# Kernel optimization log

Hardware: AMD Instinct MI355X
Metric: run time of the kernel (lower is better)

The kernel has to match this reference:

```python
import jax, jax.numpy as jnp
import numpy as np

B, T, D = 4, 2048, 2048
H, HD = 16, 128  # n_heads, head_dim; inner_dim = H*HD = 2048
SCALE = float(np.sqrt(HD))


def setup_inputs() -> dict:
    key = jax.random.key(0)
    kx, kq, kk, kv, ko = jax.random.split(key, 5)
    s = 0.02
    return {
        "x":  jax.random.normal(kx, (B, T, D), jnp.float32),
        "Wq": jax.random.normal(kq, (D, H * HD), jnp.float32) * s,
        "Wk": jax.random.normal(kk, (D, H * HD), jnp.float32) * s,
        "Wv": jax.random.normal(kv, (D, H * HD), jnp.float32) * s,
        "Wo": jax.random.normal(ko, (H * HD, D), jnp.float32) * s,
        "layer_idx": 0,
    }


def reference(x, Wq, Wk, Wv, Wo, layer_idx):
    # Cache starts empty and T <= max_cache_size, so cached_k/v == k/v and
    # T_cache == T; the sink/window mask reduces to a standard causal mask.
    b, t, _ = x.shape

    def split_heads(y):
        return y.reshape(b, t, H, HD).transpose(0, 2, 1, 3)  # (B,H,T,HD)

    q = split_heads(x @ Wq)
    k = split_heads(x @ Wk)
    v = split_heads(x @ Wv)

    scores = jnp.einsum('bhqd,bhkd->bhqk', q, k) / SCALE  # (B,H,T,T)
    q_idx = jnp.arange(t)
    k_idx = jnp.arange(t)
    causal = k_idx[None, :] <= q_idx[:, None]  # T_cache - T + q_idx == q_idx
    scores = jnp.where(causal[None, None], scores, -jnp.inf)
    w = jax.nn.softmax(scores, axis=-1)
    out = jnp.einsum('bhqk,bhkd->bhqd', w, v)
    out = out.transpose(0, 2, 1, 3).reshape(b, t, H * HD)
    return out @ Wo
```

## Files before the change

kernel.cpp:

```cpp
#include <hip/hip_runtime.h>
#include <hip/hip_bf16.h>
#include <stdint.h>

#define TT   2048
#define DD   2048
#define NH   16
#define NB   4
#define HDIM 128
#define MSZ  (NB * TT)
#define NQKV (3 * DD)
#define NT   32

typedef __attribute__((ext_vector_type(8))) __bf16 bf16x8;
typedef __attribute__((ext_vector_type(4))) float  f32x4;

typedef __attribute__((address_space(3))) void       lds_void;
typedef const __attribute__((address_space(1))) void g_void;

__device__ inline unsigned short f2bf(float f) {
  union { float f; unsigned u; } v; v.f = f;
  unsigned r = v.u + 0x7fffu + ((v.u >> 16) & 1u);
  return (unsigned short)(r >> 16);
}

__device__ inline unsigned short bfc(float f) {
  return __builtin_bit_cast(unsigned short, (__bf16)f);
}

__device__ inline void gload16(const void* g, void* l) {
  __builtin_amdgcn_global_load_lds((g_void*)g, (lds_void*)l, 16, 0, 0);
}

__device__ inline f32x4 mfma16(bf16x8 a, bf16x8 b, f32x4 c) {
  return __builtin_amdgcn_mfma_f32_16x16x32_bf16(a, b, c, 0, 0, 0);
}

#define RORMAX(x, C)                                                        \
  do {                                                                      \
    int pi_ = __builtin_amdgcn_mov_dpp(__builtin_bit_cast(int, x), (C),     \
                                       0xF, 0xF, true);                     \
    x = fmaxf(x, __builtin_bit_cast(float, pi_));                           \
  } while (0)

__global__ __launch_bounds__(256) void cvtx(const float* __restrict__ x,
                                            unsigned short* __restrict__ xb) {
  const int n4 = MSZ * DD / 4;
  for (int i = blockIdx.x * blockDim.x + threadIdx.x; i < n4;
       i += gridDim.x * blockDim.x) {
    float4 v = ((const float4*)x)[i];
    uint2 u;
    u.x = (unsigned)f2bf(v.x) | ((unsigned)f2bf(v.y) << 16);
    u.y = (unsigned)f2bf(v.z) | ((unsigned)f2bf(v.w) << 16);
    *(uint2*)&xb[(size_t)i * 4] = u;
  }
}

__global__ __launch_bounds__(256) void transW(const float* __restrict__ Wq,
                                              const float* __restrict__ Wk,
                                              const float* __restrict__ Wv,
                                              const float* __restrict__ Wo,
                                              unsigned short* __restrict__ Wtq,
                                              unsigned short* __restrict__ Wto) {
  __shared__ float tl[32][33];
  const int z = blockIdx.z;
  const float* W = (z == 0) ? Wq : (z == 1) ? Wk : (z == 2) ? Wv : Wo;
  unsigned short* outp = (z < 3) ? (Wtq + (size_t)z * DD * DD) : Wto;
  const int c = threadIdx.x & 31, r8 = threadIdx.x >> 5;
  const int k0 = blockIdx.y * 32, n0 = blockIdx.x * 32;
#pragma unroll
  for (int i = 0; i < 4; ++i)
    tl[r8 + 8 * i][c] = W[(size_t)(k0 + r8 + 8 * i) * DD + n0 + c];
  __syncthreads();
#pragma unroll
  for (int i = 0; i < 4; ++i)
    outp[(size_t)(n0 + r8 + 8 * i) * DD + k0 + c] = f2bf(tl[c][r8 + 8 * i]);
}

template <int EPI>
__global__ __launch_bounds__(512, 2) void gemm8(
    const unsigned short* __restrict__ A, const unsigned short* __restrict__ Bt,
    unsigned short* __restrict__ Qb, unsigned short* __restrict__ Kb,
    unsigned short* __restrict__ Vt, float* __restrict__ Cf) {
  __shared__ __align__(16) unsigned short As[2][2][8192];
  __shared__ __align__(16) unsigned short Bs[2][2][8192];
  const int tid = threadIdx.x;
  const int lane = tid & 63;
  const int w = tid >> 6;
  const int wm = w >> 2, wn = w & 3;
  const int l15 = lane & 15, g = lane >> 4;
  const int m0 = blockIdx.y * 256, n0 = blockIdx.x * 256;

  const int u  = (tid * 16) ^ (((tid >> 5) & 1) << 5);
  const int sr = (u >> 6) & 127;
  const int sc = (u & 63) >> 1;
  const unsigned short* sA0 = A  + (size_t)(m0 + sr) * DD + sc;
  const unsigned short* sA1 = A  + (size_t)(m0 + 128 + sr) * DD + sc;
  const unsigned short* sB0 = Bt + (size_t)(n0 + sr) * DD + sc;
  const unsigned short* sB1 = Bt + (size_t)(n0 + 128 + sr) * DD + sc;

  const int pA = ((l15 * 64 + g * 16) ^ (((l15 >> 3) & 1) << 5)) >> 1;
  const int pB = (wn & 1) * 2048 + pA;

  f32x4 acc[8][4] = {};

#define STAGE(kt, hf)                                                         \
  do {                                                                        \
    if ((kt) < NT) {                                                          \
      const unsigned short* s_ = (hf) == 0 ? sA0 : (hf) == 1 ? sA1            \
                                 : (hf) == 2 ? sB0 : sB1;                     \
      s_ += (kt) * 64;                                                        \
      unsigned short* d_ = ((hf) < 2 ? &As[(kt) & 1][(hf) & 1][0]             \
                                     : &Bs[(kt) & 1][(hf) & 1][0]) + tid * 8; \
      gload16(s_, d_);                                                        \
      gload16(s_ + 32, d_ + 4096);                                            \
    }                                                                         \
  } while (0)

#define MFMAQ(q)                                                              \
  do {                                                                        \
    __builtin_amdgcn_s_setprio(1);                                            \
    _Pragma("unroll") for (int n2 = 0; n2 < 2; ++n2)                          \
    _Pragma("unroll") for (int m2 = 0; m2 < 4; ++m2)                          \
    _Pragma("unroll") for (int kk = 0; kk < 2; ++kk)                          \
      acc[((q) & 1) * 4 + m2][((q) >> 1) * 2 + n2] =                          \
          mfma16(af[((q) & 1) * 4 + m2][kk], bq[((q) >> 1) * 2 + n2][kk],     \
                 acc[((q) & 1) * 4 + m2][((q) >> 1) * 2 + n2]);               \
    __builtin_amdgcn_s_setprio(0);                                            \
  } while (0)

#define TILE(t, buf)                                                          \
  do {                                                                        \
    const unsigned short* Ab = &As[buf][wm][0];                               \
    const unsigned short* Bb = &Bs[buf][wn >> 1][0];                          \
    bf16x8 af[8][2], bq[4][2];                                                \
    _Pragma("unroll") for (int m = 0; m < 8; ++m) {                           \
      af[m][0] = *(const bf16x8*)&Ab[pA + m * 512];                           \
      af[m][1] = *(const bf16x8*)&Ab[pA + m * 512 + 4096];                    \
    }                                                                         \
    _Pragma("unroll") for (int n = 0; n < 4; ++n) {                           \
      bq[n][0] = *(const bf16x8*)&Bb[pB + n * 512];                           \
      bq[n][1] = *(const bf16x8*)&Bb[pB + n * 512 + 4096];                    \
    }                                                                         \
    STAGE((t) + 1, 3);                                                        \
    __builtin_amdgcn_s_barrier();                                             \
    MFMAQ(0);                                                                 \
    asm volatile("s_waitcnt lgkmcnt(0)" ::: "memory");                        \
    __builtin_amdgcn_sched_barrier(0);                                        \
    __builtin_amdgcn_s_barrier();                                             \
    STAGE((t) + 2, 0);                                                        \
    __builtin_amdgcn_s_barrier();                                             \
    MFMAQ(1);                                                                 \
    __builtin_amdgcn_s_barrier();                                             \
    STAGE((t) + 2, 1);                                                        \
    __builtin_amdgcn_s_barrier();                                             \
    MFMAQ(2);                                                                 \
    __builtin_amdgcn_s_barrier();                                             \
    STAGE((t) + 2, 2);                                                        \
    __builtin_amdgcn_s_barrier();                                             \
    MFMAQ(3);                                                                 \
    asm volatile("s_waitcnt vmcnt(6)" ::: "memory");                          \
    __builtin_amdgcn_sched_barrier(0);                                        \
    __builtin_amdgcn_s_barrier();                                             \
  } while (0)

  STAGE(0, 0); STAGE(0, 1); STAGE(0, 2); STAGE(0, 3);
  STAGE(1, 0); STAGE(1, 1); STAGE(1, 2);
  asm volatile("s_waitcnt vmcnt(6)" ::: "memory");
  __builtin_amdgcn_sched_barrier(0);
  __builtin_amdgcn_s_barrier();

#pragma unroll 1
  for (int it = 0; it < NT / 2; ++it) {
    TILE(2 * it, 0);
    TILE(2 * it + 1, 1);
  }
#undef TILE
#undef MFMAQ
#undef STAGE

  const float QSCALE = 0.1275174308f;
#pragma unroll
  for (int m = 0; m < 8; ++m) {
#pragma unroll
    for (int n = 0; n < 4; ++n) {
      const int row0 = m0 + wm * 128 + m * 16 + 4 * g;
      const int col2 = wn * 64 + n * 16;
      const int col = n0 + col2 + l15;
      if (EPI == 1) {
#pragma unroll
        for (int r = 0; r < 4; ++r)
          Cf[(size_t)(row0 + r) * DD + col] = acc[m][n][r];
      } else {
        const int mat = n0 >> 11;
        const int h = ((n0 & 2047) + col2) >> 7;
        const int hd = (col2 & 127) + l15;
        if (mat == 0) {
#pragma unroll
          for (int r = 0; r < 4; ++r) {
            const int mm = row0 + r, b = mm >> 11, t = mm & 2047;
            Qb[((size_t)(b * NH + h) * TT + t) * HDIM + hd] =
                f2bf(acc[m][n][r] * QSCALE);
          }
        } else if (mat == 1) {
#pragma unroll
          for (int r = 0; r < 4; ++r) {
            const int mm = row0 + r, b = mm >> 11, t = mm & 2047;
            Kb[((size_t)(b * NH + h) * TT + t) * HDIM + hd] = f2bf(acc[m][n][r]);
          }
        } else {
          const int b = row0 >> 11, t = row0 & 2047;
          uint2 uu;
          uu.x = (unsigned)f2bf(acc[m][n][0]) | ((unsigned)f2bf(acc[m][n][1]) << 16);
          uu.y = (unsigned)f2bf(acc[m][n][2]) | ((unsigned)f2bf(acc[m][n][3]) << 16);
          *(uint2*)&Vt[((size_t)(b * NH + h) * HDIM + hd) * TT + t] = uu;
        }
      }
    }
  }
}

__global__ __launch_bounds__(256, 4) void attn(const unsigned short* __restrict__ Qb,
                                               const unsigned short* __restrict__ Kb,
                                               const unsigned short* __restrict__ Vt,
                                               unsigned short* __restrict__ O) {
  __shared__ __align__(16) unsigned short Ks[2][4096];
  __shared__ __align__(16) unsigned short Vs[2][4096];
  __shared__ __align__(16) unsigned short pl[4][16][40];

  const int bid = blockIdx.x;
  const int bx = (bid >> 3) & 15;
  const int bh = (bid & 7) + 8 * (bid >> 7);
  const int tid = threadIdx.x;
  const int w = tid >> 6;
  const int lane = tid & 63;
  const int l15 = lane & 15, g = lane >> 4;

  const unsigned short* Qh = Qb + (size_t)bh * TT * HDIM;
  const unsigned short* Kh = Kb + (size_t)bh * TT * HDIM;
  const unsigned short* Vh = Vt + (size_t)bh * HDIM * TT;
  const int b = bh >> 4, h = bh & 15;

  bf16x8 ones;
#pragma unroll
  for (int i = 0; i < 8; ++i) ones[i] = (__bf16)1.0f;

  const int kch = tid >> 5, krow = tid & 31;
  const int vc = tid >> 7, vrow = tid & 127;

  int buf = 0;
#pragma unroll 1
  for (int ph = 0; ph < 2; ++ph) {
    const int qt = ph ? bx : (31 - bx);
    const int q0 = qt * 64 + w * 16;
    const int nt = 2 * qt + 2;

    bf16x8 qf[4];
#pragma unroll
    for (int kc = 0; kc < 4; ++kc)
      qf[kc] = *(const bf16x8*)&Qh[(size_t)(q0 + l15) * HDIM + kc * 32 + g * 8];

    f32x4 o[8] = {};
    float mrow[4], lrow[4];
#pragma unroll
    for (int r = 0; r < 4; ++r) { mrow[r] = -1e30f; lrow[r] = 0.f; }

    {
      const int kv0 = 0;
      gload16(Kh + (size_t)(kv0 + krow) * HDIM + kch * 8,      &Ks[buf][(kch * 32 + krow) * 8]);
      gload16(Kh + (size_t)(kv0 + krow) * HDIM + (kch + 8) * 8,&Ks[buf][((kch + 8) * 32 + krow) * 8]);
      gload16(Vh + (size_t)vrow * TT + kv0 + vc * 8,           &Vs[buf][(vc * 128 + vrow) * 8]);
      gload16(Vh + (size_t)vrow * TT + kv0 + (vc + 2) * 8,     &Vs[buf][((vc + 2) * 128 + vrow) * 8]);
    }

#pragma unroll 1
    for (int t = 0; t < nt; ++t) {
      const int kv0 = t * 32;
      __syncthreads();
      if (t + 1 < nt) {
        const int kvn = kv0 + 32;
        gload16(Kh + (size_t)(kvn + krow) * HDIM + kch * 8,      &Ks[buf ^ 1][(kch * 32 + krow) * 8]);
        gload16(Kh + (size_t)(kvn + krow) * HDIM + (kch + 8) * 8,&Ks[buf ^ 1][((kch + 8) * 32 + krow) * 8]);
        gload16(Vh + (size_t)vrow * TT + kvn + vc * 8,           &Vs[buf ^ 1][(vc * 128 + vrow) * 8]);
        gload16(Vh + (size_t)vrow * TT + kvn + (vc + 2) * 8,     &Vs[buf ^ 1][((vc + 2) * 128 + vrow) * 8]);
      }

      if (kv0 <= q0 + 15) {
        f32x4 s0 = {}, s1 = {};
#pragma unroll
        for (int kc = 0; kc < 4; ++kc) {
          bf16x8 k0 = *(const bf16x8*)&Ks[buf][((kc * 4 + g) * 32 + l15) * 8];
          bf16x8 k1 = *(const bf16x8*)&Ks[buf][((kc * 4 + g) * 32 + 16 + l15) * 8];
          s0 = mfma16(qf[kc], k0, s0);
          s1 = mfma16(qf[kc], k1, s1);
        }
        float pmax[4];
#pragma unroll
        for (int r = 0; r < 4; ++r) {
          const int q = q0 + 4 * g + r;
          if (kv0 + l15 > q) s0[r] = -1e30f;
          if (kv0 + 16 + l15 > q) s1[r] = -1e30f;
          pmax[r] = fmaxf(s0[r], s1[r]);
        }
#pragma unroll
        for (int r = 0; r < 4; ++r) {
          RORMAX(pmax[r], 0x121);
          RORMAX(pmax[r], 0x122);
          RORMAX(pmax[r], 0x124);
          RORMAX(pmax[r], 0x128);
        }
        int need = 0;
#pragma unroll
        for (int r = 0; r < 4; ++r) need |= (pmax[r] > mrow[r] + 12.0f);
        if (__any(need)) {
          float al[4];
#pragma unroll
          for (int r = 0; r < 4; ++r) {
            const float mn = fmaxf(mrow[r], pmax[r]);
            al[r] = __builtin_amdgcn_exp2f(mrow[r] - mn);
            mrow[r] = mn;
            lrow[r] *= al[r];
          }
#pragma unroll
          for (int n8 = 0; n8 < 8; ++n8)
#pragma unroll
            for (int r = 0; r < 4; ++r) o[n8][r] *= al[r];
        }
#pragma unroll
        for (int r = 0; r < 4; ++r) {
          s0[r] = __builtin_amdgcn_exp2f(s0[r] - mrow[r]);
          s1[r] = __builtin_amdgcn_exp2f(s1[r] - mrow[r]);
        }

#pragma unroll
        for (int r = 0; r < 4; ++r) {
          pl[w][4 * g + r][l15] = bfc(s0[r]);
          pl[w][4 * g + r][16 + l15] = bfc(s1[r]);
        }
        bf16x8 pf = *(const bf16x8*)&pl[w][l15][g * 8];
        f32x4 z = {};
        f32x4 sm = mfma16(pf, ones, z);
#pragma unroll
        for (int r = 0; r < 4; ++r) lrow[r] += sm[r];
#pragma unroll
        for (int n8 = 0; n8 < 8; ++n8) {
          bf16x8 vf = *(const bf16x8*)&Vs[buf][(g * 128 + n8 * 16 + l15) * 8];
          o[n8] = mfma16(pf, vf, o[n8]);
        }
      }
      __syncthreads();
      buf ^= 1;
    }

    float linv[4];
#pragma unroll
    for (int r = 0; r < 4; ++r) linv[r] = 1.0f / lrow[r];
#pragma unroll
    for (int n8 = 0; n8 < 8; ++n8) {
#pragma unroll
      for (int r = 0; r < 4; ++r) {
        const int q = q0 + 4 * g + r;
        O[((size_t)(b * TT + q)) * (NH * HDIM) + h * HDIM + n8 * 16 + l15] =
            f2bf(o[n8][r] * linv[r]);
      }
    }
  }
}

extern "C" void kernel_launch(void* const* d_in, const int* in_sizes, int n_in,
                              void* d_out, int out_size, void* d_ws, size_t ws_size,
                              hipStream_t stream) {
  const float* x  = (const float*)d_in[0];
  const float* Wq = (const float*)d_in[1];
  const float* Wk = (const float*)d_in[2];
  const float* Wv = (const float*)d_in[3];
  const float* Wo = (const float*)d_in[4];
  float* out = (float*)d_out;

  char* ws = (char*)d_ws;
  size_t off = 0;
  unsigned short* xb  = (unsigned short*)(ws + off); off += (size_t)MSZ * DD * 2;
  unsigned short* Wtq = (unsigned short*)(ws + off); off += (size_t)NQKV * DD * 2;
  unsigned short* Wto = (unsigned short*)(ws + off); off += (size_t)DD * DD * 2;
  unsigned short* Qb  = (unsigned short*)(ws + off); off += (size_t)MSZ * DD * 2;
  unsigned short* Kb  = (unsigned short*)(ws + off); off += (size_t)MSZ * DD * 2;
  unsigned short* Vt  = (unsigned short*)(ws + off); off += (size_t)MSZ * DD * 2;
  unsigned short* Ob  = xb;

  cvtx<<<2048, 256, 0, stream>>>(x, xb);
  transW<<<dim3(64, 64, 4), 256, 0, stream>>>(Wq, Wk, Wv, Wo, Wtq, Wto);
  gemm8<0><<<dim3(NQKV / 256, MSZ / 256), 512, 0, stream>>>(xb, Wtq, Qb, Kb, Vt, nullptr);
  attn<<<1024, 256, 0, stream>>>(Qb, Kb, Vt, Ob);
  gemm8<1><<<dim3(DD / 256, MSZ / 256), 512, 0, stream>>>(Ob, Wto, nullptr, nullptr, nullptr, out);
}
```

Measured before the change: 574.8 us.

## Swizzle GEMM block mapping, split LDS fragment loads around MFMA, drain tail

The two GEMMs now use a 1D grid whose block index is remapped so that the 8 XCD-interleaved blocks map to contiguous row bands, which should improve L2 reuse per chiplet. Inside each k-tile, only half of the A/B fragments are read from LDS before the first MFMA quarter, and the rest are issued while it runs, overlapping LDS latency with compute. The MFMA loop order puts kk outermost. The last two tiles use a full vmcnt(0) wait instead of vmcnt(6). These add complexity to the schedule and assume grid sizes divisible by the swizzle pattern.

After: 558.7 us. 1.03x faster.

```diff
diff --git a/kernel.cpp b/kernel.cpp
--- a/kernel.cpp
+++ b/kernel.cpp
@@ -76,7 +76,7 @@
     outp[(size_t)(n0 + r8 + 8 * i) * DD + k0 + c] = f2bf(tl[c][r8 + 8 * i]);
 }
 
-template <int EPI>
+template <int EPI, int GX>
 __global__ __launch_bounds__(512, 2) void gemm8(
     const unsigned short* __restrict__ A, const unsigned short* __restrict__ Bt,
     unsigned short* __restrict__ Qb, unsigned short* __restrict__ Kb,
@@ -88,7 +88,9 @@
   const int w = tid >> 6;
   const int wm = w >> 2, wn = w & 3;
   const int l15 = lane & 15, g = lane >> 4;
-  const int m0 = blockIdx.y * 256, n0 = blockIdx.x * 256;
+  const int bid = blockIdx.x;
+  const int swz = (bid & 7) * (GX * 4) + (bid >> 3);
+  const int m0 = (swz / GX) * 256, n0 = (swz % GX) * 256;
 
   const int u  = (tid * 16) ^ (((tid >> 5) & 1) << 5);
   const int sr = (u >> 6) & 127;
@@ -116,37 +118,44 @@
     }                                                                         \
   } while (0)
 
+#define LDA(m)                                                                \
+  do {                                                                        \
+    af[m][0] = *(const bf16x8*)&Ab[pA + (m) * 512];                           \
+    af[m][1] = *(const bf16x8*)&Ab[pA + (m) * 512 + 4096];                    \
+  } while (0)
+#define LDB(n)                                                                \
+  do {                                                                        \
+    bq[n][0] = *(const bf16x8*)&Bb[pB + (n) * 512];                           \
+    bq[n][1] = *(const bf16x8*)&Bb[pB + (n) * 512 + 4096];                    \
+  } while (0)
+
 #define MFMAQ(q)                                                              \
   do {                                                                        \
     __builtin_amdgcn_s_setprio(1);                                            \
+    _Pragma("unroll") for (int kk = 0; kk < 2; ++kk)                          \
     _Pragma("unroll") for (int n2 = 0; n2 < 2; ++n2)                          \
     _Pragma("unroll") for (int m2 = 0; m2 < 4; ++m2)                          \
-    _Pragma("unroll") for (int kk = 0; kk < 2; ++kk)                          \
       acc[((q) & 1) * 4 + m2][((q) >> 1) * 2 + n2] =                          \
           mfma16(af[((q) & 1) * 4 + m2][kk], bq[((q) >> 1) * 2 + n2][kk],     \
                  acc[((q) & 1) * 4 + m2][((q) >> 1) * 2 + n2]);               \
     __builtin_amdgcn_s_setprio(0);                                            \
   } while (0)
 
-#define TILE(t, buf)                                                          \
+#define TILE(t, buf, VM)                                                      \
   do {                                                                        \
     const unsigned short* Ab = &As[buf][wm][0];                               \
     const unsigned short* Bb = &Bs[buf][wn >> 1][0];                          \
     bf16x8 af[8][2], bq[4][2];                                                \
-    _Pragma("unroll") for (int m = 0; m < 8; ++m) {                           \
-      af[m][0] = *(const bf16x8*)&Ab[pA + m * 512];                           \
-      af[m][1] = *(const bf16x8*)&Ab[pA + m * 512 + 4096];                    \
-    }                                                                         \
-    _Pragma("unroll") for (int n = 0; n < 4; ++n) {                           \
-      bq[n][0] = *(const bf16x8*)&Bb[pB + n * 512];                           \
-      bq[n][1] = *(const bf16x8*)&Bb[pB + n * 512 + 4096];                    \
-    }                                                                         \
+    LDA(0); LDA(1); LDA(2); LDA(3);                                           \
+    LDB(0); LDB(1);                                                           \
     STAGE((t) + 1, 3);                                                        \
     __builtin_amdgcn_s_barrier();                                             \
-    MFMAQ(0);                                                                 \
+    MFMAQ(0);                      \
+    LDA(4); LDA(5); LDA(6); LDA(7);                                           \
+    LDB(2); LDB(3);                                                           \
     asm volatile("s_waitcnt lgkmcnt(0)" ::: "memory");                        \
     __builtin_amdgcn_sched_barrier(0);                                        \
-    __builtin_amdgcn_s_barrier();                                             \
+    __builtin_amdgcn_s_barrier();    \
     STAGE((t) + 2, 0);                                                        \
     __builtin_amdgcn_s_barrier();                                             \
     MFMAQ(1);                                                                 \
@@ -158,7 +167,10 @@
     STAGE((t) + 2, 2);                                                        \
     __builtin_amdgcn_s_barrier();                                             \
     MFMAQ(3);                                                                 \
-    asm volatile("s_waitcnt vmcnt(6)" ::: "memory");                          \
+    if (VM)                                                                   \
+      asm volatile("s_waitcnt vmcnt(6)" ::: "memory");                        \
+    else                                                                      \
+      asm volatile("s_waitcnt vmcnt(0)" ::: "memory");                        \
     __builtin_amdgcn_sched_barrier(0);                                        \
     __builtin_amdgcn_s_barrier();                                             \
   } while (0)
@@ -170,12 +182,16 @@
   __builtin_amdgcn_s_barrier();
 
 #pragma unroll 1
-  for (int it = 0; it < NT / 2; ++it) {
-    TILE(2 * it, 0);
-    TILE(2 * it + 1, 1);
+  for (int it = 0; it < NT / 2 - 1; ++it) {
+    TILE(2 * it, 0, 6);
+    TILE(2 * it + 1, 1, 6);
   }
+  TILE(NT - 2, 0, 0);
+  TILE(NT - 1, 1, 0);
 #undef TILE
 #undef MFMAQ
+#undef LDB
+#undef LDA
 #undef STAGE
 
   const float QSCALE = 0.1275174308f;
@@ -388,7 +404,7 @@
 
   cvtx<<<2048, 256, 0, stream>>>(x, xb);
   transW<<<dim3(64, 64, 4), 256, 0, stream>>>(Wq, Wk, Wv, Wo, Wtq, Wto);
-  gemm8<0><<<dim3(NQKV / 256, MSZ / 256), 512, 0, stream>>>(xb, Wtq, Qb, Kb, Vt, nullptr);
+  gemm8<0, 24><<<768, 512, 0, stream>>>(xb, Wtq, Qb, Kb, Vt, nullptr);
   attn<<<1024, 256, 0, stream>>>(Qb, Kb, Vt, Ob);
-  gemm8<1><<<dim3(DD / 256, MSZ / 256), 512, 0, stream>>>(Ob, Wto, nullptr, nullptr, nullptr, out);
-}
+  gemm8<1, 8><<<256, 512, 0, stream>>>(Ob, Wto, nullptr, nullptr, nullptr, out);
+}
```
